# Kernel tuning notes

Hardware: AMD Instinct MI355X
Metric: run time of the kernel (lower is better)

The kernel has to match this reference:

```python
import jax, jax.numpy as jnp
import numpy as np

E, K = 8, 2
B, S, H = 8, 2048, 512
R0, R1, O = 256, 256, 512
T = B * S


def _make_routing(key):
    # Mixtral-style: top-k softmax weights [T, K] and one-hot mask [E, K, T]
    k1, k2 = jax.random.split(key)
    sel = jax.random.randint(k1, (T, K), 0, E)                      # selected expert per (token, slot)
    rw = jax.nn.softmax(jax.random.normal(k2, (T, K)), axis=-1)
    mask = jax.nn.one_hot(sel, E, dtype=jnp.bool_)                  # [T, K, E]
    mask = jnp.transpose(mask, (2, 1, 0))                           # [E, K, T]
    return mask, rw


def setup_inputs() -> dict:
    key = jax.random.key(0)
    ks = jax.random.split(key, 10)
    x = jax.random.normal(ks[0], (B, S, H), dtype=jnp.float32)
    m1, rw1 = _make_routing(ks[1])
    m2, rw2 = _make_routing(ks[2])
    m3, rw3 = _make_routing(ks[3])
    s = 0.02
    W1 = jax.random.normal(ks[4], (E, R0, H), dtype=jnp.float32) * s
    b1 = jnp.zeros((E, R0), dtype=jnp.float32)
    W2 = jax.random.normal(ks[5], (E, R1, R0), dtype=jnp.float32) * s
    b2 = jnp.zeros((E, R1), dtype=jnp.float32)
    W3 = jax.random.normal(ks[6], (E, O, R1), dtype=jnp.float32) * s
    b3 = jnp.zeros((E, O), dtype=jnp.float32)
    return {"x": x,
            "expert_mask1": m1, "expert_mask2": m2, "expert_mask3": m3,
            "routing_weights1": rw1, "routing_weights2": rw2, "routing_weights3": rw3,
            "W1": W1, "b1": b1, "W2": W2, "b2": b2, "W3": W3, "b3": b3}


def _moe_stage(h, mask, rw, W, b, act):
    # combine[e, t] = routing weight of token t for expert e (0 if not routed)
    cmb = jnp.einsum('ekt,tk->et', mask.astype(h.dtype), rw)
    acc0 = jnp.zeros((h.shape[0], W.shape[1]), dtype=h.dtype)

    def body(acc, ew):
        Wi, bi, ci = ew            # Wi: [out, in], bi: [out], ci: [T]
        out = h @ Wi.T + bi
        if act:
            out = jax.nn.relu(out)
        return acc + ci[:, None] * out, None

    acc, _ = jax.lax.scan(body, acc0, (W, b, cmb))
    return acc


def reference(x, expert_mask1, expert_mask2, expert_mask3,
              routing_weights1, routing_weights2, routing_weights3,
              W1, b1, W2, b2, W3, b3):
    bsz, seq, dim = x.shape
    h = x.reshape(-1, dim)                                          # [T, H]
    h = _moe_stage(h, expert_mask1, routing_weights1, W1, b1, act=False)   # [T, R0]
    h = _moe_stage(h, expert_mask2, routing_weights2, W2, b2, act=False)   # [T, R1]
    h = _moe_stage(h, expert_mask3, routing_weights3, W3, b3, act=True)    # relu on expert output, then combine
    out = jax.nn.relu(h.reshape(bsz, seq, -1))
    return out
```

## Files before the change

kernel.cpp:

```cpp
#include <hip/hip_runtime.h>

#define T_TOKENS 16384
#define CAP 12288
#define CNT_STRIDE 16

typedef unsigned short u16;
typedef unsigned int u32;
typedef __attribute__((ext_vector_type(8))) short short8;
typedef __attribute__((ext_vector_type(4))) float float4v;

__device__ __forceinline__ u16 f2b(float f) {
  unsigned u = __float_as_uint(f);
  u = (u + 0x7fffu + ((u >> 16) & 1u)) >> 16;
  return (u16)u;
}
__device__ __forceinline__ float b2f(u16 h) {
  return __uint_as_float(((unsigned)h) << 16);
}

__device__ __forceinline__ void gl_lds16(const u16* g, u16* l) {
  __builtin_amdgcn_global_load_lds((const __attribute__((address_space(1))) u32*)g,
                                   (__attribute__((address_space(3))) u32*)l, 16, 0, 0);
}

__global__ void convert_all(const float* __restrict__ x, const float* __restrict__ W1,
                            const float* __restrict__ W2, const float* __restrict__ W3,
                            u16* __restrict__ xb, u16* __restrict__ Wb1,
                            u16* __restrict__ Wb2, u16* __restrict__ Wb3,
                            int* __restrict__ cnt) {
  if (blockIdx.x == 0 && threadIdx.x < 24) cnt[threadIdx.x * CNT_STRIDE] = 0;
  const int nx = T_TOKENS * 512, n1 = 8 * 256 * 512, n2 = 8 * 256 * 256;
  int base = (blockIdx.x * 256 + threadIdx.x) * 8;
  const float* src; u16* dst; int off = base;
  if (base < nx) { src = x; dst = xb; }
  else if (base < nx + n1) { src = W1; dst = Wb1; off = base - nx; }
  else if (base < nx + n1 + n2) { src = W2; dst = Wb2; off = base - nx - n1; }
  else { src = W3; dst = Wb3; off = base - nx - n1 - n2; }
  float4 a0 = *(const float4*)(src + off);
  float4 a1 = *(const float4*)(src + off + 4);
  short8 v;
  v[0] = (short)f2b(a0.x); v[1] = (short)f2b(a0.y);
  v[2] = (short)f2b(a0.z); v[3] = (short)f2b(a0.w);
  v[4] = (short)f2b(a1.x); v[5] = (short)f2b(a1.y);
  v[6] = (short)f2b(a1.z); v[7] = (short)f2b(a1.w);
  *(short8*)(dst + off) = v;
}

__global__ void route_kernel(const int* __restrict__ m1, const int* __restrict__ m2,
                             const int* __restrict__ m3, const float* __restrict__ rw1,
                             const float* __restrict__ rw2, const float* __restrict__ rw3,
                             int* __restrict__ cnt, int* __restrict__ idxbuf,
                             float* __restrict__ wgtbuf) {
  __shared__ int lcnt[24];
  __shared__ int lbase[24];
  const int tid = threadIdx.x;
  const int t = blockIdx.x * 256 + tid;
  if (tid < 24) lcnt[tid] = 0;
  __syncthreads();

  const int* masks[3] = {m1, m2, m3};
  const float* rws[3] = {rw1, rw2, rw3};
  int expert[3][2], lpos[3][2];
#pragma unroll
  for (int s = 0; s < 3; ++s)
#pragma unroll
    for (int k = 0; k < 2; ++k) {
      int e = 0;
#pragma unroll
      for (int j = 0; j < 8; ++j)
        if (masks[s][(j * 2 + k) * T_TOKENS + t] != 0) e = j;
      expert[s][k] = e;
      lpos[s][k] = atomicAdd(&lcnt[s * 8 + e], 1);
    }
  __syncthreads();
  if (tid < 24) lbase[tid] = atomicAdd(&cnt[tid * CNT_STRIDE], lcnt[tid]);
  __syncthreads();
#pragma unroll
  for (int s = 0; s < 3; ++s)
#pragma unroll
    for (int k = 0; k < 2; ++k) {
      int e = expert[s][k];
      int p = lbase[s * 8 + e] + lpos[s][k];
      if (p < CAP) {
        idxbuf[(s * 8 + e) * CAP + p] = t * 2 + k;
        wgtbuf[(s * 8 + e) * CAP + p] = rws[s][t * 2 + k];
      }
    }
}

template <int KDIM, int NDIM_TOTAL, int SRC, int RELU>
__global__ __launch_bounds__(256, 2) void moe_gemm(
    const u16* __restrict__ Asrc, const u16* __restrict__ Wb, const float* __restrict__ bias,
    const int* __restrict__ cnt, const int* __restrict__ idxbuf, const float* __restrict__ wgtbuf,
    u16* __restrict__ outTmp) {
  __shared__ __align__(16) u16 As[128 * 64];
  __shared__ __align__(16) u16 Bs[256 * 64];
  __shared__ int rowTok[128];
  __shared__ float rowW[128];

  int b = blockIdx.x;
  int e = -1, row0 = 0, n_e = 0, accb = 0;
#pragma unroll
  for (int j = 0; j < 8; ++j) {
    int nj = cnt[j * CNT_STRIDE];
    nj = nj > CAP ? CAP : nj;
    int nb = (nj + 127) >> 7;
    if (e < 0 && b < accb + nb) { e = j; row0 = (b - accb) << 7; n_e = nj; }
    accb += nb;
  }
  if (e < 0) return;

  const int tid = threadIdx.x;
  if (tid < 128) {
    int g = row0 + tid;
    bool ok = g < n_e;
    rowTok[tid] = ok ? idxbuf[e * CAP + g] : 0;
    rowW[tid] = ok ? wgtbuf[e * CAP + g] : 0.f;
  }
  __syncthreads();

  const int nbase = blockIdx.y * 256;
  const int wv = tid >> 6, lane = tid & 63;
  const int lrow = lane & 15, lquad = lane >> 4;
  const int mh = wv >> 1, nh = wv & 1;

  const u16* Wbe = Wb + ((size_t)e * NDIM_TOTAL + nbase) * KDIM;

  const int lr = lane >> 3;
  const int lgl = (lane & 7) ^ lr;
  const u16* gB = Wbe + (size_t)(wv * 8 + lr) * KDIM + lgl * 8;
  u16* lB = &Bs[(wv * 8) * 64];
  u16* lA = &As[(wv * 8) * 64];

  const u16* gA[4];
  const u16* ga0[4];
  int awoff[4];
  if (SRC == 0) {
#pragma unroll
    for (int i = 0; i < 4; ++i) {
      int r = i * 32 + wv * 8 + lr;
      gA[i] = Asrc + (size_t)(rowTok[r] >> 1) * KDIM + lgl * 8;
    }
  } else {
#pragma unroll
    for (int i = 0; i < 4; ++i) {
      int r = i * 32 + (tid >> 3);
      ga0[i] = Asrc + (size_t)(rowTok[r] >> 1) * 2 * KDIM + (tid & 7) * 8;
      awoff[i] = (r * 8 + ((tid & 7) ^ ((tid >> 3) & 7))) * 8;
    }
  }

  float4v acc[4][8];
#pragma unroll
  for (int mt = 0; mt < 4; ++mt)
#pragma unroll
    for (int nt = 0; nt < 8; ++nt) acc[mt][nt] = (float4v)0.f;

  for (int kb = 0; kb < KDIM; kb += 64) {
#pragma unroll
    for (int i = 0; i < 8; ++i)
      gl_lds16(gB + (size_t)i * 32 * KDIM + kb, lB + i * 32 * 64);
    if (SRC == 0) {
#pragma unroll
      for (int i = 0; i < 4; ++i)
        gl_lds16(gA[i] + kb, lA + i * 32 * 64);
    } else {
#pragma unroll
      for (int i = 0; i < 4; ++i) {
        short8 v0 = *(const short8*)(ga0[i] + kb);
        short8 v1 = *(const short8*)(ga0[i] + kb + KDIM);
        short8 v;
#pragma unroll
        for (int j = 0; j < 8; ++j)
          v[j] = (short)f2b(b2f((u16)v0[j]) + b2f((u16)v1[j]));
        *(short8*)&As[awoff[i]] = v;
      }
    }
    __syncthreads();
#pragma unroll
    for (int ks = 0; ks < 64; ks += 32) {
      const int gb = ks >> 3;
      short8 af[4], bf[8];
#pragma unroll
      for (int mt = 0; mt < 4; ++mt) {
        int r = mh * 64 + mt * 16 + lrow;
        int p = (gb + lquad) ^ (lrow & 7);
        af[mt] = *(const short8*)&As[(r * 8 + p) * 8];
      }
#pragma unroll
      for (int nt = 0; nt < 8; ++nt) {
        int r = nh * 128 + nt * 16 + lrow;
        int p = (gb + lquad) ^ (lrow & 7);
        bf[nt] = *(const short8*)&Bs[(r * 8 + p) * 8];
      }
#pragma unroll
      for (int mt = 0; mt < 4; ++mt)
#pragma unroll
        for (int nt = 0; nt < 8; ++nt)
          acc[mt][nt] = __builtin_amdgcn_mfma_f32_16x16x32_bf16(af[mt], bf[nt], acc[mt][nt], 0, 0, 0);
    }
    __syncthreads();
  }

  float bv[8];
#pragma unroll
  for (int nt = 0; nt < 8; ++nt)
    bv[nt] = bias[e * NDIM_TOTAL + nbase + nh * 128 + nt * 16 + lrow];
#pragma unroll
  for (int mt = 0; mt < 4; ++mt)
#pragma unroll
    for (int i = 0; i < 4; ++i) {
      int m = mh * 64 + mt * 16 + lquad * 4 + i;
      if (row0 + m < n_e) {
        float w = rowW[m];
        size_t drow = (size_t)rowTok[m] * NDIM_TOTAL + nbase + nh * 128;
#pragma unroll
        for (int nt = 0; nt < 8; ++nt) {
          float v = acc[mt][nt][i] + bv[nt];
          if (RELU) v = fmaxf(v, 0.f);
          outTmp[drow + nt * 16 + lrow] = f2b(v * w);
        }
      }
    }
}

__global__ void finalize_kernel(const u16* __restrict__ tmp3, float* __restrict__ out) {
  int f = (blockIdx.x * 256 + threadIdx.x) * 8;
  int t = f >> 9;
  int o = f & 511;
  const u16* p = tmp3 + (size_t)t * 1024 + o;
  short8 v0 = *(const short8*)p;
  short8 v1 = *(const short8*)(p + 512);
  float4 r0, r1;
  r0.x = fmaxf(b2f((u16)v0[0]) + b2f((u16)v1[0]), 0.f);
  r0.y = fmaxf(b2f((u16)v0[1]) + b2f((u16)v1[1]), 0.f);
  r0.z = fmaxf(b2f((u16)v0[2]) + b2f((u16)v1[2]), 0.f);
  r0.w = fmaxf(b2f((u16)v0[3]) + b2f((u16)v1[3]), 0.f);
  r1.x = fmaxf(b2f((u16)v0[4]) + b2f((u16)v1[4]), 0.f);
  r1.y = fmaxf(b2f((u16)v0[5]) + b2f((u16)v1[5]), 0.f);
  r1.z = fmaxf(b2f((u16)v0[6]) + b2f((u16)v1[6]), 0.f);
  r1.w = fmaxf(b2f((u16)v0[7]) + b2f((u16)v1[7]), 0.f);
  *(float4*)(out + f) = r0;
  *(float4*)(out + f + 4) = r1;
}

extern "C" void kernel_launch(void* const* d_in, const int* in_sizes, int n_in,
                              void* d_out, int out_size, void* d_ws, size_t ws_size,
                              hipStream_t stream) {
  const float* x  = (const float*)d_in[0];
  const int* m1   = (const int*)d_in[1];
  const int* m2   = (const int*)d_in[2];
  const int* m3   = (const int*)d_in[3];
  const float* rw1 = (const float*)d_in[4];
  const float* rw2 = (const float*)d_in[5];
  const float* rw3 = (const float*)d_in[6];
  const float* W1 = (const float*)d_in[7];
  const float* b1 = (const float*)d_in[8];
  const float* W2 = (const float*)d_in[9];
  const float* b2 = (const float*)d_in[10];
  const float* W3 = (const float*)d_in[11];
  const float* b3 = (const float*)d_in[12];
  float* out = (float*)d_out;

  char* ws = (char*)d_ws;
  size_t off = 0;
  int* cnt = (int*)(ws + off); off += 24 * CNT_STRIDE * 4;
  u16* xb  = (u16*)(ws + off); off += (size_t)T_TOKENS * 512 * 2;
  u16* Wb1 = (u16*)(ws + off); off += (size_t)8 * 256 * 512 * 2;
  u16* Wb2 = (u16*)(ws + off); off += (size_t)8 * 256 * 256 * 2;
  u16* Wb3 = (u16*)(ws + off); off += (size_t)8 * 512 * 256 * 2;
  u16* tmp1 = (u16*)(ws + off); off += (size_t)T_TOKENS * 2 * 256 * 2;
  u16* tmp2 = (u16*)(ws + off); off += (size_t)T_TOKENS * 2 * 256 * 2;
  u16* tmp3 = (u16*)(ws + off); off += (size_t)T_TOKENS * 2 * 512 * 2;
  int* idxb = (int*)(ws + off); off += (size_t)3 * 8 * CAP * 4;
  float* wgtb = (float*)(ws + off); off += (size_t)3 * 8 * CAP * 4;

  convert_all<<<5376, 256, 0, stream>>>(x, W1, W2, W3, xb, Wb1, Wb2, Wb3, cnt);
  route_kernel<<<64, 256, 0, stream>>>(m1, m2, m3, rw1, rw2, rw3, cnt, idxb, wgtb);

  moe_gemm<512, 256, 0, 0><<<dim3(264, 1), 256, 0, stream>>>(
      xb, Wb1, b1, cnt + 0, idxb + 0, wgtb + 0, tmp1);
  moe_gemm<256, 256, 1, 0><<<dim3(264, 1), 256, 0, stream>>>(
      tmp1, Wb2, b2, cnt + 8 * CNT_STRIDE, idxb + 8 * CAP, wgtb + 8 * CAP, tmp2);
  moe_gemm<256, 512, 1, 1><<<dim3(264, 2), 256, 0, stream>>>(
      tmp2, Wb3, b3, cnt + 16 * CNT_STRIDE, idxb + 16 * CAP, wgtb + 16 * CAP, tmp3);

  finalize_kernel<<<4096, 256, 0, stream>>>(tmp3, out);
}
```

Before: 197.4 us.

## Fuse x bf16 conversion into first GEMM load and merge routing with weight conversion

Drops the separate fp32-to-bf16 conversion pass over x. The first GEMM now reads fp32 activations directly, converts them to bf16 in registers and stores them swizzled into LDS. Routing and weight conversion are merged into one prep kernel, and the counter reset moves to a memset. This avoids writing and re-reading a 16 MB bf16 copy of x and removes one launch, at the cost of losing async global-to-LDS loads for A in stage 1. Because tokens are routed to two experts, stage 1 also reads each x row twice in fp32.

```diff
diff --git a/kernel.cpp b/kernel.cpp
--- a/kernel.cpp
+++ b/kernel.cpp
@@ -23,74 +23,70 @@
                                    (__attribute__((address_space(3))) u32*)l, 16, 0, 0);
 }
 
-__global__ void convert_all(const float* __restrict__ x, const float* __restrict__ W1,
-                            const float* __restrict__ W2, const float* __restrict__ W3,
-                            u16* __restrict__ xb, u16* __restrict__ Wb1,
-                            u16* __restrict__ Wb2, u16* __restrict__ Wb3,
-                            int* __restrict__ cnt) {
-  if (blockIdx.x == 0 && threadIdx.x < 24) cnt[threadIdx.x * CNT_STRIDE] = 0;
-  const int nx = T_TOKENS * 512, n1 = 8 * 256 * 512, n2 = 8 * 256 * 256;
-  int base = (blockIdx.x * 256 + threadIdx.x) * 8;
-  const float* src; u16* dst; int off = base;
-  if (base < nx) { src = x; dst = xb; }
-  else if (base < nx + n1) { src = W1; dst = Wb1; off = base - nx; }
-  else if (base < nx + n1 + n2) { src = W2; dst = Wb2; off = base - nx - n1; }
-  else { src = W3; dst = Wb3; off = base - nx - n1 - n2; }
-  float4 a0 = *(const float4*)(src + off);
-  float4 a1 = *(const float4*)(src + off + 4);
-  short8 v;
-  v[0] = (short)f2b(a0.x); v[1] = (short)f2b(a0.y);
-  v[2] = (short)f2b(a0.z); v[3] = (short)f2b(a0.w);
-  v[4] = (short)f2b(a1.x); v[5] = (short)f2b(a1.y);
-  v[6] = (short)f2b(a1.z); v[7] = (short)f2b(a1.w);
-  *(short8*)(dst + off) = v;
-}
-
-__global__ void route_kernel(const int* __restrict__ m1, const int* __restrict__ m2,
-                             const int* __restrict__ m3, const float* __restrict__ rw1,
-                             const float* __restrict__ rw2, const float* __restrict__ rw3,
-                             int* __restrict__ cnt, int* __restrict__ idxbuf,
-                             float* __restrict__ wgtbuf) {
-  __shared__ int lcnt[24];
-  __shared__ int lbase[24];
+__global__ __launch_bounds__(256) void prep_kernel(
+    const int* __restrict__ m1, const int* __restrict__ m2, const int* __restrict__ m3,
+    const float* __restrict__ rw1, const float* __restrict__ rw2, const float* __restrict__ rw3,
+    const float* __restrict__ W1, const float* __restrict__ W2, const float* __restrict__ W3,
+    u16* __restrict__ Wb1, u16* __restrict__ Wb2, u16* __restrict__ Wb3,
+    int* __restrict__ cnt, int* __restrict__ idxbuf, float* __restrict__ wgtbuf) {
   const int tid = threadIdx.x;
-  const int t = blockIdx.x * 256 + tid;
-  if (tid < 24) lcnt[tid] = 0;
-  __syncthreads();
-
-  const int* masks[3] = {m1, m2, m3};
-  const float* rws[3] = {rw1, rw2, rw3};
-  int expert[3][2], lpos[3][2];
-#pragma unroll
-  for (int s = 0; s < 3; ++s)
-#pragma unroll
-    for (int k = 0; k < 2; ++k) {
-      int e = 0;
-#pragma unroll
-      for (int j = 0; j < 8; ++j)
-        if (masks[s][(j * 2 + k) * T_TOKENS + t] != 0) e = j;
-      expert[s][k] = e;
-      lpos[s][k] = atomicAdd(&lcnt[s * 8 + e], 1);
-    }
-  __syncthreads();
-  if (tid < 24) lbase[tid] = atomicAdd(&cnt[tid * CNT_STRIDE], lcnt[tid]);
-  __syncthreads();
-#pragma unroll
-  for (int s = 0; s < 3; ++s)
-#pragma unroll
-    for (int k = 0; k < 2; ++k) {
-      int e = expert[s][k];
-      int p = lbase[s * 8 + e] + lpos[s][k];
-      if (p < CAP) {
-        idxbuf[(s * 8 + e) * CAP + p] = t * 2 + k;
-        wgtbuf[(s * 8 + e) * CAP + p] = rws[s][t * 2 + k];
-      }
-    }
+  const int bid = blockIdx.x;
+  if (bid < 64) {
+    __shared__ int lcnt[24];
+    __shared__ int lbase[24];
+    if (tid < 24) lcnt[tid] = 0;
+    __syncthreads();
+    const int t = bid * 256 + tid;
+    const int* masks[3] = {m1, m2, m3};
+    const float* rws[3] = {rw1, rw2, rw3};
+    int expert[3][2], lpos[3][2];
+#pragma unroll
+    for (int s = 0; s < 3; ++s)
+#pragma unroll
+      for (int k = 0; k < 2; ++k) {
+        int e = 0;
+#pragma unroll
+        for (int j = 0; j < 8; ++j)
+          if (masks[s][(j * 2 + k) * T_TOKENS + t] != 0) e = j;
+        expert[s][k] = e;
+        lpos[s][k] = atomicAdd(&lcnt[s * 8 + e], 1);
+      }
+    __syncthreads();
+    if (tid < 24) lbase[tid] = atomicAdd(&cnt[tid * CNT_STRIDE], lcnt[tid]);
+    __syncthreads();
+#pragma unroll
+    for (int s = 0; s < 3; ++s)
+#pragma unroll
+      for (int k = 0; k < 2; ++k) {
+        int e = expert[s][k];
+        int p = lbase[s * 8 + e] + lpos[s][k];
+        if (p < CAP) {
+          idxbuf[(s * 8 + e) * CAP + p] = t * 2 + k;
+          wgtbuf[(s * 8 + e) * CAP + p] = rws[s][t * 2 + k];
+        }
+      }
+  } else {
+    for (int j = bid - 64; j < 1280; j += 192) {
+      int base = j * 2048 + tid * 8;
+      const float* src; u16* dst; int off = base;
+      if (base < 1048576) { src = W1; dst = Wb1; }
+      else if (base < 1572864) { src = W2; dst = Wb2; off = base - 1048576; }
+      else { src = W3; dst = Wb3; off = base - 1572864; }
+      float4 a0 = *(const float4*)(src + off);
+      float4 a1 = *(const float4*)(src + off + 4);
+      short8 v;
+      v[0] = (short)f2b(a0.x); v[1] = (short)f2b(a0.y);
+      v[2] = (short)f2b(a0.z); v[3] = (short)f2b(a0.w);
+      v[4] = (short)f2b(a1.x); v[5] = (short)f2b(a1.y);
+      v[6] = (short)f2b(a1.z); v[7] = (short)f2b(a1.w);
+      *(short8*)(dst + off) = v;
+    }
+  }
 }
 
 template <int KDIM, int NDIM_TOTAL, int SRC, int RELU>
 __global__ __launch_bounds__(256, 2) void moe_gemm(
-    const u16* __restrict__ Asrc, const u16* __restrict__ Wb, const float* __restrict__ bias,
+    const void* __restrict__ Asrc_, const u16* __restrict__ Wb, const float* __restrict__ bias,
     const int* __restrict__ cnt, const int* __restrict__ idxbuf, const float* __restrict__ wgtbuf,
     u16* __restrict__ outTmp) {
   __shared__ __align__(16) u16 As[128 * 64];
@@ -130,24 +126,18 @@
   const int lgl = (lane & 7) ^ lr;
   const u16* gB = Wbe + (size_t)(wv * 8 + lr) * KDIM + lgl * 8;
   u16* lB = &Bs[(wv * 8) * 64];
-  u16* lA = &As[(wv * 8) * 64];
-
-  const u16* gA[4];
-  const u16* ga0[4];
+
+  const float* ga_f[4];
+  const u16* ga_b[4];
   int awoff[4];
-  if (SRC == 0) {
-#pragma unroll
-    for (int i = 0; i < 4; ++i) {
-      int r = i * 32 + wv * 8 + lr;
-      gA[i] = Asrc + (size_t)(rowTok[r] >> 1) * KDIM + lgl * 8;
-    }
-  } else {
-#pragma unroll
-    for (int i = 0; i < 4; ++i) {
-      int r = i * 32 + (tid >> 3);
-      ga0[i] = Asrc + (size_t)(rowTok[r] >> 1) * 2 * KDIM + (tid & 7) * 8;
-      awoff[i] = (r * 8 + ((tid & 7) ^ ((tid >> 3) & 7))) * 8;
-    }
+#pragma unroll
+  for (int i = 0; i < 4; ++i) {
+    int r = i * 32 + (tid >> 3);
+    if (SRC == 0)
+      ga_f[i] = (const float*)Asrc_ + (size_t)(rowTok[r] >> 1) * KDIM + (tid & 7) * 8;
+    else
+      ga_b[i] = (const u16*)Asrc_ + (size_t)(rowTok[r] >> 1) * 2 * KDIM + (tid & 7) * 8;
+    awoff[i] = (r * 8 + ((tid & 7) ^ (r & 7))) * 8;
   }
 
   float4v acc[4][8];
@@ -162,17 +152,25 @@
       gl_lds16(gB + (size_t)i * 32 * KDIM + kb, lB + i * 32 * 64);
     if (SRC == 0) {
 #pragma unroll
-      for (int i = 0; i < 4; ++i)
-        gl_lds16(gA[i] + kb, lA + i * 32 * 64);
+      for (int i = 0; i < 4; ++i) {
+        float4 a0 = *(const float4*)(ga_f[i] + kb);
+        float4 a1 = *(const float4*)(ga_f[i] + kb + 4);
+        short8 v;
+        v[0] = (short)f2b(a0.x); v[1] = (short)f2b(a0.y);
+        v[2] = (short)f2b(a0.z); v[3] = (short)f2b(a0.w);
+        v[4] = (short)f2b(a1.x); v[5] = (short)f2b(a1.y);
+        v[6] = (short)f2b(a1.z); v[7] = (short)f2b(a1.w);
+        *(short8*)&As[awoff[i]] = v;
+      }
     } else {
 #pragma unroll
       for (int i = 0; i < 4; ++i) {
-        short8 v0 = *(const short8*)(ga0[i] + kb);
-        short8 v1 = *(const short8*)(ga0[i] + kb + KDIM);
+        short8 v0 = *(const short8*)(ga_b[i] + kb);
+        short8 v1 = *(const short8*)(ga_b[i] + kb + KDIM);
         short8 v;
 #pragma unroll
-        for (int j = 0; j < 8; ++j)
-          v[j] = (short)f2b(b2f((u16)v0[j]) + b2f((u16)v1[j]));
+        for (int jj = 0; jj < 8; ++jj)
+          v[jj] = (short)f2b(b2f((u16)v0[jj]) + b2f((u16)v1[jj]));
         *(short8*)&As[awoff[i]] = v;
       }
     }
@@ -265,7 +263,6 @@
   char* ws = (char*)d_ws;
   size_t off = 0;
   int* cnt = (int*)(ws + off); off += 24 * CNT_STRIDE * 4;
-  u16* xb  = (u16*)(ws + off); off += (size_t)T_TOKENS * 512 * 2;
   u16* Wb1 = (u16*)(ws + off); off += (size_t)8 * 256 * 512 * 2;
   u16* Wb2 = (u16*)(ws + off); off += (size_t)8 * 256 * 256 * 2;
   u16* Wb3 = (u16*)(ws + off); off += (size_t)8 * 512 * 256 * 2;
@@ -275,11 +272,12 @@
   int* idxb = (int*)(ws + off); off += (size_t)3 * 8 * CAP * 4;
   float* wgtb = (float*)(ws + off); off += (size_t)3 * 8 * CAP * 4;
 
-  convert_all<<<5376, 256, 0, stream>>>(x, W1, W2, W3, xb, Wb1, Wb2, Wb3, cnt);
-  route_kernel<<<64, 256, 0, stream>>>(m1, m2, m3, rw1, rw2, rw3, cnt, idxb, wgtb);
+  hipMemsetAsync(cnt, 0, 24 * CNT_STRIDE * 4, stream);
+  prep_kernel<<<256, 256, 0, stream>>>(m1, m2, m3, rw1, rw2, rw3, W1, W2, W3,
+                                       Wb1, Wb2, Wb3, cnt, idxb, wgtb);
 
   moe_gemm<512, 256, 0, 0><<<dim3(264, 1), 256, 0, stream>>>(
-      xb, Wb1, b1, cnt + 0, idxb + 0, wgtb + 0, tmp1);
+      x, Wb1, b1, cnt + 0, idxb + 0, wgtb + 0, tmp1);
   moe_gemm<256, 256, 1, 0><<<dim3(264, 1), 256, 0, stream>>>(
       tmp1, Wb2, b2, cnt + 8 * CNT_STRIDE, idxb + 8 * CAP, wgtb + 8 * CAP, tmp2);
   moe_gemm<256, 512, 1, 1><<<dim3(264, 2), 256, 0, stream>>>(
```

After: 193.1 us. 2.2% less time.
